# Optimization experiments

Measured on AMD Instinct MI355X. Metric: run time of the kernel, lower is better.

The kernel has to match this reference:

```python
import jax, jax.numpy as jnp
import numpy as np

N, D, IN_DIM, H, L = 20000, 32, 3, 64, 3


def _lstm_agg(h_nodes, nbr_sorted, W_ih, W_hh, b_ih, b_hh):
    """Batched LSTM over each node's (sorted) neighbor sequence; returns final hidden state h_T."""
    n = h_nodes.shape[0]
    hidden = W_hh.shape[1]

    def step(carry, idx):
        h, c = carry
        x = h_nodes[idx]                                     # [N, in_d] irregular gather
        gates = x @ W_ih.T + h @ W_hh.T + b_ih + b_hh        # [N, 4H], torch gate order i,f,g,o
        i_g, f_g, g_g, o_g = jnp.split(gates, 4, axis=-1)
        c = jax.nn.sigmoid(f_g) * c + jax.nn.sigmoid(i_g) * jnp.tanh(g_g)
        h = jax.nn.sigmoid(o_g) * jnp.tanh(c)
        return (h, c), None

    init = (jnp.zeros((n, hidden), h_nodes.dtype), jnp.zeros((n, hidden), h_nodes.dtype))
    (h_T, _), _ = jax.lax.scan(step, init, nbr_sorted.T)      # scan over D neighbor slots
    return h_T


def _layer(h, nbr_sorted, W_ih, W_hh, b_ih, b_hh, Wl, bl):
    agg = _lstm_agg(h, nbr_sorted, W_ih, W_hh, b_ih, b_hh)    # [N, H]
    comb = jnp.concatenate([h, agg], axis=-1)                 # [N, in_d + H]
    return jax.nn.relu(comb @ Wl.T + bl)


def _forward(node_features, nbr, params, W_out, b_out):
    nbr_sorted = jnp.sort(nbr, axis=1)   # permutation-invariant ordering (Eq. 9)
    h = node_features
    for p in params:
        h = _layer(h, nbr_sorted, *p)
    return (h @ W_out.T + b_out).squeeze(-1)   # [N] per-node log-likelihood scores


def setup_inputs():
    key = jax.random.key(0)
    ks = jax.random.split(key, 40)
    inp = {}
    inp["node_features"] = jax.random.normal(ks[0], (N, IN_DIM), jnp.float32)
    inp["nbr"] = jax.random.randint(ks[1], (N, D), 0, N, jnp.int32)
    k = 2
    s = 1.0 / np.sqrt(H)
    for l in range(L):
        in_d = IN_DIM if l == 0 else H
        inp[f"W_ih{l}"] = (jax.random.normal(ks[k], (4 * H, in_d)) * (1.0 / np.sqrt(in_d))).astype(jnp.float32); k += 1
        inp[f"W_hh{l}"] = (jax.random.normal(ks[k], (4 * H, H)) * s).astype(jnp.float32); k += 1
        inp[f"b_ih{l}"] = (jax.random.normal(ks[k], (4 * H,)) * s).astype(jnp.float32); k += 1
        inp[f"b_hh{l}"] = (jax.random.normal(ks[k], (4 * H,)) * s).astype(jnp.float32); k += 1
        inp[f"Wl{l}"] = (jax.random.normal(ks[k], (H, in_d + H)) * (1.0 / np.sqrt(in_d + H))).astype(jnp.float32); k += 1
        inp[f"bl{l}"] = (jax.random.normal(ks[k], (H,)) * s).astype(jnp.float32); k += 1
    inp["W_out"] = (jax.random.normal(ks[k], (1, H)) * s).astype(jnp.float32); k += 1
    inp["b_out"] = jnp.zeros((1,), jnp.float32)
    return inp


def reference(node_features, nbr, W_ih0, W_hh0, b_ih0, b_hh0, Wl0, bl0, W_ih1, W_hh1, b_ih1, b_hh1, Wl1, bl1, W_ih2, W_hh2, b_ih2, b_hh2, Wl2, bl2, W_out, b_out):
    params = [
        (W_ih0, W_hh0, b_ih0, b_hh0, Wl0, bl0),
        (W_ih1, W_hh1, b_ih1, b_hh1, Wl1, bl1),
        (W_ih2, W_hh2, b_ih2, b_hh2, Wl2, bl2),
    ]
    return _forward(node_features, nbr, params, W_out, b_out)
```

## Files before the change

kernel.cpp:

```cpp
#include <hip/hip_runtime.h>
#include <hip/hip_bf16.h>

#define NN 20000
#define NG 1250
#define LOG2E 1.44269504088896f
#define TWOLOG2E 2.88539008177793f

typedef __attribute__((ext_vector_type(8))) short short8;
typedef __attribute__((ext_vector_type(4))) float floatx4;

__device__ __forceinline__ floatx4 MF(short8 a, short8 b, floatx4 c) {
    return __builtin_amdgcn_mfma_f32_16x16x32_bf16(a, b, c, 0, 0, 0);
}
__device__ __forceinline__ float ex2(float x) { return __builtin_amdgcn_exp2f(x); }
__device__ __forceinline__ float rcp(float x) { return __builtin_amdgcn_rcpf(x); }
__device__ __forceinline__ unsigned short bf16r(float x) {
    return __builtin_bit_cast(unsigned short, __float2bfloat16(x));
}
__device__ __forceinline__ void lds_barrier() {
    asm volatile("s_waitcnt lgkmcnt(0)\n\ts_barrier" ::: "memory");
}
__device__ __forceinline__ int rowswz(int L) {
    return L ^ (((L >> 4) & 1) << 1) ^ ((L >> 3) & 1);
}

__global__ void sort_nbrs_kernel(const int* __restrict__ nbr, int* __restrict__ nbrT) {
    int n = blockIdx.x * blockDim.x + threadIdx.x;
    if (n >= NN) return;
    int v[32];
    const int4* src = (const int4*)(nbr + n * 32);
    #pragma unroll
    for (int i = 0; i < 8; i++) {
        int4 t = src[i];
        v[4*i] = t.x; v[4*i+1] = t.y; v[4*i+2] = t.z; v[4*i+3] = t.w;
    }
    #pragma unroll
    for (int k = 2; k <= 32; k <<= 1)
        #pragma unroll
        for (int j = k >> 1; j > 0; j >>= 1)
            #pragma unroll
            for (int i = 0; i < 32; i++) {
                int ixj = i ^ j;
                if (ixj > i) {
                    bool up = (i & k) == 0;
                    int a = v[i], b = v[ixj];
                    bool sw = up ? (a > b) : (a < b);
                    if (sw) { v[i] = b; v[ixj] = a; }
                }
            }
    int g = n >> 4, m = n & 15;
    int base = g * 512 + m;
    #pragma unroll
    for (int t = 0; t < 32; t++) nbrT[base + t * 16] = v[t];
}

#define PREP_TOT (49152 + 49152 + 12288 + 12288 + 768 + 640000)
__global__ void prep_kernel(const float* __restrict__ x,
    const float* __restrict__ Wih0, const float* __restrict__ Whh0,
    const float* __restrict__ bih0, const float* __restrict__ bhh0, const float* __restrict__ Wl0,
    const float* __restrict__ Wih1, const float* __restrict__ Whh1,
    const float* __restrict__ bih1, const float* __restrict__ bhh1, const float* __restrict__ Wl1,
    const float* __restrict__ Wih2, const float* __restrict__ Whh2,
    const float* __restrict__ bih2, const float* __restrict__ bhh2, const float* __restrict__ Wl2,
    unsigned short* __restrict__ Wih_p, unsigned short* __restrict__ Whh_p,
    unsigned short* __restrict__ Wlx_p, unsigned short* __restrict__ Wlh_p,
    float* __restrict__ bsum, unsigned short* __restrict__ x32)
{
    for (int i = blockIdx.x * 256 + threadIdx.x; i < PREP_TOT; i += gridDim.x * 256) {
        int j = i;
        if (j < 49152) {
            int l = j >> 14, e = j & 16383;
            if (l == 0) {
                if (e < 8192) {
                    int col = e >> 5, k = e & 31;
                    float sc = (col >= 128 && col < 192) ? TWOLOG2E : LOG2E;
                    float v = (k < 3) ? Wih0[col*3 + k] * sc : 0.f;
                    Wih_p[e] = bf16r(v);
                }
            } else {
                int col = e >> 6, k = e & 63;
                const float* W = (l == 1) ? Wih1 : Wih2;
                float sc = (col >= 128 && col < 192) ? TWOLOG2E : LOG2E;
                Wih_p[l*16384 + e] = bf16r(W[col*64 + k] * sc);
            }
            continue;
        }
        j -= 49152;
        if (j < 49152) {
            int l = j >> 14, e = j & 16383;
            int col = e >> 6, k = e & 63;
            const float* W = (l == 0) ? Whh0 : ((l == 1) ? Whh1 : Whh2);
            float sc = (col >= 128 && col < 192) ? TWOLOG2E : LOG2E;
            Whh_p[l*16384 + e] = bf16r(W[col*64 + k] * sc);
            continue;
        }
        j -= 49152;
        if (j < 12288) {
            int l = j >> 12, e = j & 4095;
            if (l == 0) {
                if (e < 2048) {
                    int col = e >> 5, k = e & 31;
                    float v = (k < 3) ? Wl0[col*67 + k] : 0.f;
                    Wlx_p[e] = bf16r(v);
                }
            } else {
                int col = e >> 6, k = e & 63;
                const float* W = (l == 1) ? Wl1 : Wl2;
                Wlx_p[l*4096 + e] = bf16r(W[col*128 + k]);
            }
            continue;
        }
        j -= 12288;
        if (j < 12288) {
            int l = j >> 12, e = j & 4095;
            int col = e >> 6, k = e & 63;
            float v = (l == 0) ? Wl0[col*67 + 3 + k]
                               : ((l == 1) ? Wl1 : Wl2)[col*128 + 64 + k];
            Wlh_p[l*4096 + e] = bf16r(v);
            continue;
        }
        j -= 12288;
        if (j < 768) {
            int l = j >> 8, col = j & 255;
            const float* bi = (l == 0) ? bih0 : ((l == 1) ? bih1 : bih2);
            const float* bh = (l == 0) ? bhh0 : ((l == 1) ? bhh1 : bhh2);
            float sc = (col >= 128 && col < 192) ? TWOLOG2E : LOG2E;
            bsum[l*256 + col] = (bi[col] + bh[col]) * sc;
            continue;
        }
        j -= 768;
        {
            int n = j >> 5, k = j & 31;
            x32[j] = bf16r((k < 3) ? x[n*3 + k] : 0.f);
        }
    }
}

template<int XKC, int LASTL>
__global__ __launch_bounds__(256, 3)
void lstm_mfma_kernel(const unsigned short* __restrict__ xsrc,
                      const int* __restrict__ nbrT,
                      const unsigned short* __restrict__ Wih,
                      const unsigned short* __restrict__ Whh,
                      const float* __restrict__ bsum,
                      const unsigned short* __restrict__ Wlx,
                      const unsigned short* __restrict__ Wlh,
                      const float* __restrict__ bl,
                      const float* __restrict__ W_out,
                      const float* __restrict__ b_out,
                      void* __restrict__ hout)
{
    __shared__ unsigned short sA[2][1024];
    __shared__ float sRed[64];

    const int w    = threadIdx.x >> 6;
    const int lane = threadIdx.x & 63;
    const int q    = lane >> 4;
    const int c    = lane & 15;
    const int XS   = XKC * 32;

    const int g = blockIdx.x;
    const int node0 = g * 16;
    const int* nbg = nbrT + g * 512;

    short8 fWih[4][XKC];
    short8 fWhh[4][2];
    float  biasv[4];
    #pragma unroll
    for (int t4 = 0; t4 < 4; t4++) {
        int col = 64*t4 + 16*w + c;
        biasv[t4] = bsum[col];
        #pragma unroll
        for (int kc = 0; kc < XKC; kc++)
            fWih[t4][kc] = *(const short8*)(Wih + col*XS + kc*32 + q*8);
        #pragma unroll
        for (int kc = 0; kc < 2; kc++)
            fWhh[t4][kc] = *(const short8*)(Whh + col*64 + kc*32 + q*8);
    }

    float cst[4] = {0.f, 0.f, 0.f, 0.f};
    short8 hA[2] = {};

    int idx_cur = nbg[c];
    int idx_nxt = nbg[16 + c];
    short8 xg[XKC];
    #pragma unroll
    for (int kc = 0; kc < XKC; kc++)
        xg[kc] = *(const short8*)(xsrc + (long)idx_cur * XS + kc*32 + q*8);

    #pragma unroll 1
    for (int t = 0; t < 32; t++) {
        floatx4 acc[4];
        #pragma unroll
        for (int t4 = 0; t4 < 4; t4++) {
            floatx4 a; a[0] = biasv[t4]; a[1] = biasv[t4]; a[2] = biasv[t4]; a[3] = biasv[t4];
            acc[t4] = a;
        }
        if (t > 0) {
            #pragma unroll
            for (int t4 = 0; t4 < 4; t4++) {
                acc[t4] = MF(hA[0], fWhh[t4][0], acc[t4]);
                acc[t4] = MF(hA[1], fWhh[t4][1], acc[t4]);
            }
        }
        #pragma unroll
        for (int t4 = 0; t4 < 4; t4++)
            #pragma unroll
            for (int kc = 0; kc < XKC; kc++)
                acc[t4] = MF(xg[kc], fWih[t4][kc], acc[t4]);

        if (t < 31) {
            #pragma unroll
            for (int kc = 0; kc < XKC; kc++)
                xg[kc] = *(const short8*)(xsrc + (long)idx_nxt * XS + kc*32 + q*8);
            int tn = (t + 2 < 32) ? t + 2 : 31;
            idx_nxt = nbg[tn*16 + c];
        }

        unsigned short* sAb = sA[t & 1];
        const int u = 16*w + c;
        #pragma unroll
        for (int r = 0; r < 4; r++) {
            float gi = acc[0][r], gf = acc[1][r], gg = acc[2][r], go = acc[3][r];
            float ei = ex2(-gi);
            float ef = ex2(-gf);
            float eo = ex2(-go);
            float eg = ex2(-__builtin_fabsf(gg));
            float iG = __builtin_copysignf(1.f - eg, gg) * rcp((1.f + ei) * (1.f + eg));
            float cm = fmaf(cst[r], rcp(1.f + ef), iG);
            cst[r] = cm;
            float ec = ex2(-TWOLOG2E * __builtin_fabsf(cm));
            float h  = __builtin_copysignf(1.f - ec, cm) * rcp((1.f + eo) * (1.f + ec));
            int row = (4*q + r) + 16*(u >> 3);
            sAb[rowswz(row)*8 + (u & 7)] = bf16r(h);
        }
        lds_barrier();
        hA[0] = *(const short8*)(sA[t & 1] + rowswz(lane)*8);
        hA[1] = *(const short8*)(sA[t & 1] + 512 + rowswz(lane)*8);
    }

    const int col = 16*w + c;
    short8 fx[XKC], fh[2];
    float blv = bl[col];
    #pragma unroll
    for (int kc = 0; kc < XKC; kc++)
        fx[kc] = *(const short8*)(Wlx + col*XS + kc*32 + q*8);
    fh[0] = *(const short8*)(Wlh + col*64 + q*8);
    fh[1] = *(const short8*)(Wlh + col*64 + 32 + q*8);
    short8 hin[XKC];
    #pragma unroll
    for (int kc = 0; kc < XKC; kc++)
        hin[kc] = *(const short8*)(xsrc + (long)(node0 + c) * XS + kc*32 + q*8);

    floatx4 a; a[0] = blv; a[1] = blv; a[2] = blv; a[3] = blv;
    #pragma unroll
    for (int kc = 0; kc < XKC; kc++) a = MF(hin[kc], fx[kc], a);
    a = MF(hA[0], fh[0], a);
    a = MF(hA[1], fh[1], a);

    if (!LASTL) {
        #pragma unroll
        for (int r = 0; r < 4; r++)
            ((unsigned short*)hout)[(node0 + 4*q + r) * 64 + col] = bf16r(fmaxf(a[r], 0.f));
    } else {
        float wo = W_out[col];
        float p[4];
        #pragma unroll
        for (int r = 0; r < 4; r++) p[r] = fmaxf(a[r], 0.f) * wo;
        #pragma unroll
        for (int d = 1; d < 16; d <<= 1) {
            #pragma unroll
            for (int r = 0; r < 4; r++) p[r] += __shfl_xor(p[r], d);
        }
        if (c == 0) {
            #pragma unroll
            for (int r = 0; r < 4; r++) sRed[w*16 + 4*q + r] = p[r];
        }
        lds_barrier();
        if (w == 0 && lane < 16)
            ((float*)hout)[node0 + lane] =
                sRed[lane] + sRed[16 + lane] + sRed[32 + lane] + sRed[48 + lane] + b_out[0];
    }
}

extern "C" void kernel_launch(void* const* d_in, const int* in_sizes, int n_in,
                              void* d_out, int out_size, void* d_ws, size_t ws_size,
                              hipStream_t stream) {
    (void)in_sizes; (void)n_in; (void)out_size; (void)ws_size;
    const float* node_features = (const float*)d_in[0];
    const int*   nbr           = (const int*)d_in[1];
    const float* Wih[3] = {(const float*)d_in[2],  (const float*)d_in[8],  (const float*)d_in[14]};
    const float* Whh[3] = {(const float*)d_in[3],  (const float*)d_in[9],  (const float*)d_in[15]};
    const float* bih[3] = {(const float*)d_in[4],  (const float*)d_in[10], (const float*)d_in[16]};
    const float* bhh[3] = {(const float*)d_in[5],  (const float*)d_in[11], (const float*)d_in[17]};
    const float* Wl[3]  = {(const float*)d_in[6],  (const float*)d_in[12], (const float*)d_in[18]};
    const float* bl[3]  = {(const float*)d_in[7],  (const float*)d_in[13], (const float*)d_in[19]};
    const float* W_out  = (const float*)d_in[20];
    const float* b_out  = (const float*)d_in[21];

    char* ws = (char*)d_ws;
    int*            nbrT  = (int*)ws;
    unsigned short* x32   = (unsigned short*)(ws + 2560000);
    unsigned short* hb1   = (unsigned short*)(ws + 3840000);
    unsigned short* hb2   = (unsigned short*)(ws + 6400000);
    unsigned short* Wih_p = (unsigned short*)(ws + 8960000);
    unsigned short* Whh_p = (unsigned short*)(ws + 9058304);
    unsigned short* Wlx_p = (unsigned short*)(ws + 9156608);
    unsigned short* Wlh_p = (unsigned short*)(ws + 9181184);
    float*          bsum  = (float*)(ws + 9205760);

    prep_kernel<<<1024, 256, 0, stream>>>(node_features,
        Wih[0], Whh[0], bih[0], bhh[0], Wl[0],
        Wih[1], Whh[1], bih[1], bhh[1], Wl[1],
        Wih[2], Whh[2], bih[2], bhh[2], Wl[2],
        Wih_p, Whh_p, Wlx_p, Wlh_p, bsum, x32);
    sort_nbrs_kernel<<<(NN + 255) / 256, 256, 0, stream>>>(nbr, nbrT);

    lstm_mfma_kernel<1, 0><<<NG, 256, 0, stream>>>(x32, nbrT,
        Wih_p,         Whh_p,         bsum,       Wlx_p,        Wlh_p,        bl[0],
        nullptr, nullptr, hb1);
    lstm_mfma_kernel<2, 0><<<NG, 256, 0, stream>>>(hb1, nbrT,
        Wih_p + 16384, Whh_p + 16384, bsum + 256, Wlx_p + 4096, Wlh_p + 4096, bl[1],
        nullptr, nullptr, hb2);
    lstm_mfma_kernel<2, 1><<<NG, 256, 0, stream>>>(hb2, nbrT,
        Wih_p + 32768, Whh_p + 32768, bsum + 512, Wlx_p + 8192, Wlh_p + 8192, bl[2],
        W_out, b_out, (float*)d_out);
}
```

Before: 293.4 us.

## Process two node groups per LSTM block and merge sort into prep kernel

Each LSTM block now handles two independent 16-node groups and interleaves their MFMA chains, gathers and gate math. This gives more instruction-level parallelism to hide the serial recurrence latency and halves the grid. The neighbor sort is folded into the prep kernel as extra blocks, which removes one launch. The cost is higher register pressure under launch_bounds(256,3), and with 625 blocks some CUs may be left idle.

```diff
diff --git a/kernel.cpp b/kernel.cpp
--- a/kernel.cpp
+++ b/kernel.cpp
@@ -3,8 +3,11 @@
 
 #define NN 20000
 #define NG 1250
+#define NB 625
 #define LOG2E 1.44269504088896f
 #define TWOLOG2E 2.88539008177793f
+#define SORT_BLOCKS 79
+#define PREP_BLOCKS 1024
 
 typedef __attribute__((ext_vector_type(8))) short short8;
 typedef __attribute__((ext_vector_type(4))) float floatx4;
@@ -24,38 +27,9 @@
     return L ^ (((L >> 4) & 1) << 1) ^ ((L >> 3) & 1);
 }
 
-__global__ void sort_nbrs_kernel(const int* __restrict__ nbr, int* __restrict__ nbrT) {
-    int n = blockIdx.x * blockDim.x + threadIdx.x;
-    if (n >= NN) return;
-    int v[32];
-    const int4* src = (const int4*)(nbr + n * 32);
-    #pragma unroll
-    for (int i = 0; i < 8; i++) {
-        int4 t = src[i];
-        v[4*i] = t.x; v[4*i+1] = t.y; v[4*i+2] = t.z; v[4*i+3] = t.w;
-    }
-    #pragma unroll
-    for (int k = 2; k <= 32; k <<= 1)
-        #pragma unroll
-        for (int j = k >> 1; j > 0; j >>= 1)
-            #pragma unroll
-            for (int i = 0; i < 32; i++) {
-                int ixj = i ^ j;
-                if (ixj > i) {
-                    bool up = (i & k) == 0;
-                    int a = v[i], b = v[ixj];
-                    bool sw = up ? (a > b) : (a < b);
-                    if (sw) { v[i] = b; v[ixj] = a; }
-                }
-            }
-    int g = n >> 4, m = n & 15;
-    int base = g * 512 + m;
-    #pragma unroll
-    for (int t = 0; t < 32; t++) nbrT[base + t * 16] = v[t];
-}
-
 #define PREP_TOT (49152 + 49152 + 12288 + 12288 + 768 + 640000)
-__global__ void prep_kernel(const float* __restrict__ x,
+__global__ void prep_sort_kernel(const float* __restrict__ x,
+    const int* __restrict__ nbr, int* __restrict__ nbrT,
     const float* __restrict__ Wih0, const float* __restrict__ Whh0,
     const float* __restrict__ bih0, const float* __restrict__ bhh0, const float* __restrict__ Wl0,
     const float* __restrict__ Wih1, const float* __restrict__ Whh1,
@@ -66,7 +40,39 @@
     unsigned short* __restrict__ Wlx_p, unsigned short* __restrict__ Wlh_p,
     float* __restrict__ bsum, unsigned short* __restrict__ x32)
 {
-    for (int i = blockIdx.x * 256 + threadIdx.x; i < PREP_TOT; i += gridDim.x * 256) {
+    if (blockIdx.x < SORT_BLOCKS) {
+        int n = blockIdx.x * 256 + threadIdx.x;
+        if (n >= NN) return;
+        int v[32];
+        const int4* src = (const int4*)(nbr + n * 32);
+        #pragma unroll
+        for (int i = 0; i < 8; i++) {
+            int4 t = src[i];
+            v[4*i] = t.x; v[4*i+1] = t.y; v[4*i+2] = t.z; v[4*i+3] = t.w;
+        }
+        #pragma unroll
+        for (int k = 2; k <= 32; k <<= 1)
+            #pragma unroll
+            for (int j = k >> 1; j > 0; j >>= 1)
+                #pragma unroll
+                for (int i = 0; i < 32; i++) {
+                    int ixj = i ^ j;
+                    if (ixj > i) {
+                        bool up = (i & k) == 0;
+                        int a = v[i], b = v[ixj];
+                        bool sw = up ? (a > b) : (a < b);
+                        if (sw) { v[i] = b; v[ixj] = a; }
+                    }
+                }
+        int g = n >> 4, m = n & 15;
+        int base = g * 512 + m;
+        #pragma unroll
+        for (int t = 0; t < 32; t++) nbrT[base + t * 16] = v[t];
+        return;
+    }
+
+    for (int i = (blockIdx.x - SORT_BLOCKS) * 256 + threadIdx.x; i < PREP_TOT;
+         i += PREP_BLOCKS * 256) {
         int j = i;
         if (j < 49152) {
             int l = j >> 14, e = j & 16383;
@@ -150,8 +156,8 @@
                       const float* __restrict__ b_out,
                       void* __restrict__ hout)
 {
-    __shared__ unsigned short sA[2][1024];
-    __shared__ float sRed[64];
+    __shared__ unsigned short sA[2][2][1024];
+    __shared__ float sRed[2][64];
 
     const int w    = threadIdx.x >> 6;
     const int lane = threadIdx.x & 63;
@@ -159,9 +165,9 @@
     const int c    = lane & 15;
     const int XS   = XKC * 32;
 
-    const int g = blockIdx.x;
-    const int node0 = g * 16;
-    const int* nbg = nbrT + g * 512;
+    const int g0 = blockIdx.x * 2;
+    const int node0[2] = { g0 * 16, g0 * 16 + 16 };
+    const int* nbg[2]  = { nbrT + g0 * 512, nbrT + g0 * 512 + 512 };
 
     short8 fWih[4][XKC];
     short8 fWhh[4][2];
@@ -178,65 +184,84 @@
             fWhh[t4][kc] = *(const short8*)(Whh + col*64 + kc*32 + q*8);
     }
 
-    float cst[4] = {0.f, 0.f, 0.f, 0.f};
-    short8 hA[2] = {};
-
-    int idx_cur = nbg[c];
-    int idx_nxt = nbg[16 + c];
-    short8 xg[XKC];
+    float cst[2][4] = {};
+    short8 hA[2][2] = {};
+
+    int idx_nxt[2];
+    short8 xg[2][XKC];
     #pragma unroll
-    for (int kc = 0; kc < XKC; kc++)
-        xg[kc] = *(const short8*)(xsrc + (long)idx_cur * XS + kc*32 + q*8);
+    for (int gi = 0; gi < 2; gi++) {
+        int ic = nbg[gi][c];
+        idx_nxt[gi] = nbg[gi][16 + c];
+        #pragma unroll
+        for (int kc = 0; kc < XKC; kc++)
+            xg[gi][kc] = *(const short8*)(xsrc + (long)ic * XS + kc*32 + q*8);
+    }
 
     #pragma unroll 1
     for (int t = 0; t < 32; t++) {
-        floatx4 acc[4];
-        #pragma unroll
-        for (int t4 = 0; t4 < 4; t4++) {
-            floatx4 a; a[0] = biasv[t4]; a[1] = biasv[t4]; a[2] = biasv[t4]; a[3] = biasv[t4];
-            acc[t4] = a;
-        }
+        floatx4 acc[2][4];
+        #pragma unroll
+        for (int gi = 0; gi < 2; gi++)
+            #pragma unroll
+            for (int t4 = 0; t4 < 4; t4++) {
+                floatx4 a; a[0] = biasv[t4]; a[1] = biasv[t4]; a[2] = biasv[t4]; a[3] = biasv[t4];
+                acc[gi][t4] = a;
+            }
         if (t > 0) {
             #pragma unroll
-            for (int t4 = 0; t4 < 4; t4++) {
-                acc[t4] = MF(hA[0], fWhh[t4][0], acc[t4]);
-                acc[t4] = MF(hA[1], fWhh[t4][1], acc[t4]);
-            }
+            for (int t4 = 0; t4 < 4; t4++)
+                #pragma unroll
+                for (int gi = 0; gi < 2; gi++) {
+                    acc[gi][t4] = MF(hA[gi][0], fWhh[t4][0], acc[gi][t4]);
+                    acc[gi][t4] = MF(hA[gi][1], fWhh[t4][1], acc[gi][t4]);
+                }
         }
         #pragma unroll
         for (int t4 = 0; t4 < 4; t4++)
             #pragma unroll
-            for (int kc = 0; kc < XKC; kc++)
-                acc[t4] = MF(xg[kc], fWih[t4][kc], acc[t4]);
+            for (int gi = 0; gi < 2; gi++)
+                #pragma unroll
+                for (int kc = 0; kc < XKC; kc++)
+                    acc[gi][t4] = MF(xg[gi][kc], fWih[t4][kc], acc[gi][t4]);
 
         if (t < 31) {
-            #pragma unroll
-            for (int kc = 0; kc < XKC; kc++)
-                xg[kc] = *(const short8*)(xsrc + (long)idx_nxt * XS + kc*32 + q*8);
             int tn = (t + 2 < 32) ? t + 2 : 31;
-            idx_nxt = nbg[tn*16 + c];
-        }
-
-        unsigned short* sAb = sA[t & 1];
+            #pragma unroll
+            for (int gi = 0; gi < 2; gi++) {
+                #pragma unroll
+                for (int kc = 0; kc < XKC; kc++)
+                    xg[gi][kc] = *(const short8*)(xsrc + (long)idx_nxt[gi] * XS + kc*32 + q*8);
+                idx_nxt[gi] = nbg[gi][tn*16 + c];
+            }
+        }
+
         const int u = 16*w + c;
         #pragma unroll
-        for (int r = 0; r < 4; r++) {
-            float gi = acc[0][r], gf = acc[1][r], gg = acc[2][r], go = acc[3][r];
-            float ei = ex2(-gi);
-            float ef = ex2(-gf);
-            float eo = ex2(-go);
-            float eg = ex2(-__builtin_fabsf(gg));
-            float iG = __builtin_copysignf(1.f - eg, gg) * rcp((1.f + ei) * (1.f + eg));
-            float cm = fmaf(cst[r], rcp(1.f + ef), iG);
-            cst[r] = cm;
-            float ec = ex2(-TWOLOG2E * __builtin_fabsf(cm));
-            float h  = __builtin_copysignf(1.f - ec, cm) * rcp((1.f + eo) * (1.f + ec));
-            int row = (4*q + r) + 16*(u >> 3);
-            sAb[rowswz(row)*8 + (u & 7)] = bf16r(h);
+        for (int gi = 0; gi < 2; gi++) {
+            unsigned short* sAb = &sA[gi][t & 1][0];
+            #pragma unroll
+            for (int r = 0; r < 4; r++) {
+                float gv = acc[gi][0][r], gf = acc[gi][1][r], gg = acc[gi][2][r], go = acc[gi][3][r];
+                float ei = ex2(-gv);
+                float ef = ex2(-gf);
+                float eo = ex2(-go);
+                float eg = ex2(-__builtin_fabsf(gg));
+                float iG = __builtin_copysignf(1.f - eg, gg) * rcp((1.f + ei) * (1.f + eg));
+                float cm = fmaf(cst[gi][r], rcp(1.f + ef), iG);
+                cst[gi][r] = cm;
+                float ec = ex2(-TWOLOG2E * __builtin_fabsf(cm));
+                float h  = __builtin_copysignf(1.f - ec, cm) * rcp((1.f + eo) * (1.f + ec));
+                int row = (4*q + r) + 16*(u >> 3);
+                sAb[rowswz(row)*8 + (u & 7)] = bf16r(h);
+            }
         }
         lds_barrier();
-        hA[0] = *(const short8*)(sA[t & 1] + rowswz(lane)*8);
-        hA[1] = *(const short8*)(sA[t & 1] + 512 + rowswz(lane)*8);
+        #pragma unroll
+        for (int gi = 0; gi < 2; gi++) {
+            hA[gi][0] = *(const short8*)(&sA[gi][t & 1][0] + rowswz(lane)*8);
+            hA[gi][1] = *(const short8*)(&sA[gi][t & 1][0] + 512 + rowswz(lane)*8);
+        }
     }
 
     const int col = 16*w + c;
@@ -247,39 +272,46 @@
         fx[kc] = *(const short8*)(Wlx + col*XS + kc*32 + q*8);
     fh[0] = *(const short8*)(Wlh + col*64 + q*8);
     fh[1] = *(const short8*)(Wlh + col*64 + 32 + q*8);
-    short8 hin[XKC];
+
     #pragma unroll
-    for (int kc = 0; kc < XKC; kc++)
-        hin[kc] = *(const short8*)(xsrc + (long)(node0 + c) * XS + kc*32 + q*8);
-
-    floatx4 a; a[0] = blv; a[1] = blv; a[2] = blv; a[3] = blv;
-    #pragma unroll
-    for (int kc = 0; kc < XKC; kc++) a = MF(hin[kc], fx[kc], a);
-    a = MF(hA[0], fh[0], a);
-    a = MF(hA[1], fh[1], a);
-
-    if (!LASTL) {
-        #pragma unroll
-        for (int r = 0; r < 4; r++)
-            ((unsigned short*)hout)[(node0 + 4*q + r) * 64 + col] = bf16r(fmaxf(a[r], 0.f));
-    } else {
-        float wo = W_out[col];
-        float p[4];
-        #pragma unroll
-        for (int r = 0; r < 4; r++) p[r] = fmaxf(a[r], 0.f) * wo;
-        #pragma unroll
-        for (int d = 1; d < 16; d <<= 1) {
-            #pragma unroll
-            for (int r = 0; r < 4; r++) p[r] += __shfl_xor(p[r], d);
-        }
-        if (c == 0) {
-            #pragma unroll
-            for (int r = 0; r < 4; r++) sRed[w*16 + 4*q + r] = p[r];
-        }
+    for (int gi = 0; gi < 2; gi++) {
+        short8 hin[XKC];
+        #pragma unroll
+        for (int kc = 0; kc < XKC; kc++)
+            hin[kc] = *(const short8*)(xsrc + (long)(node0[gi] + c) * XS + kc*32 + q*8);
+
+        floatx4 a; a[0] = blv; a[1] = blv; a[2] = blv; a[3] = blv;
+        #pragma unroll
+        for (int kc = 0; kc < XKC; kc++) a = MF(hin[kc], fx[kc], a);
+        a = MF(hA[gi][0], fh[0], a);
+        a = MF(hA[gi][1], fh[1], a);
+
+        if (!LASTL) {
+            #pragma unroll
+            for (int r = 0; r < 4; r++)
+                ((unsigned short*)hout)[(node0[gi] + 4*q + r) * 64 + col] = bf16r(fmaxf(a[r], 0.f));
+        } else {
+            float wo = W_out[col];
+            float p[4];
+            #pragma unroll
+            for (int r = 0; r < 4; r++) p[r] = fmaxf(a[r], 0.f) * wo;
+            #pragma unroll
+            for (int d = 1; d < 16; d <<= 1) {
+                #pragma unroll
+                for (int r = 0; r < 4; r++) p[r] += __shfl_xor(p[r], d);
+            }
+            if (c == 0) {
+                #pragma unroll
+                for (int r = 0; r < 4; r++) sRed[gi][w*16 + 4*q + r] = p[r];
+            }
+        }
+    }
+    if (LASTL) {
         lds_barrier();
-        if (w == 0 && lane < 16)
-            ((float*)hout)[node0 + lane] =
-                sRed[lane] + sRed[16 + lane] + sRed[32 + lane] + sRed[48 + lane] + b_out[0];
+        if (w < 2 && lane < 16)
+            ((float*)hout)[node0[w] + lane] =
+                sRed[w][lane] + sRed[w][16 + lane] + sRed[w][32 + lane] + sRed[w][48 + lane]
+                + b_out[0];
     }
 }
 
@@ -309,20 +341,20 @@
     unsigned short* Wlh_p = (unsigned short*)(ws + 9181184);
     float*          bsum  = (float*)(ws + 9205760);
 
-    prep_kernel<<<1024, 256, 0, stream>>>(node_features,
+    prep_sort_kernel<<<SORT_BLOCKS + PREP_BLOCKS, 256, 0, stream>>>(node_features,
+        nbr, nbrT,
         Wih[0], Whh[0], bih[0], bhh[0], Wl[0],
         Wih[1], Whh[1], bih[1], bhh[1], Wl[1],
         Wih[2], Whh[2], bih[2], bhh[2], Wl[2],
         Wih_p, Whh_p, Wlx_p, Wlh_p, bsum, x32);
-    sort_nbrs_kernel<<<(NN + 255) / 256, 256, 0, stream>>>(nbr, nbrT);
-
-    lstm_mfma_kernel<1, 0><<<NG, 256, 0, stream>>>(x32, nbrT,
+
+    lstm_mfma_kernel<1, 0><<<NB, 256, 0, stream>>>(x32, nbrT,
         Wih_p,         Whh_p,         bsum,       Wlx_p,        Wlh_p,        bl[0],
         nullptr, nullptr, hb1);
-    lstm_mfma_kernel<2, 0><<<NG, 256, 0, stream>>>(hb1, nbrT,
+    lstm_mfma_kernel<2, 0><<<NB, 256, 0, stream>>>(hb1, nbrT,
         Wih_p + 16384, Whh_p + 16384, bsum + 256, Wlx_p + 4096, Wlh_p + 4096, bl[1],
         nullptr, nullptr, hb2);
-    lstm_mfma_kernel<2, 1><<<NG, 256, 0, stream>>>(hb2, nbrT,
+    lstm_mfma_kernel<2, 1><<<NB, 256, 0, stream>>>(hb2, nbrT,
         Wih_p + 32768, Whh_p + 32768, bsum + 512, Wlx_p + 8192, Wlh_p + 8192, bl[2],
         W_out, b_out, (float*)d_out);
 }
```

Measured after the change: 332.8 us. 13.4% more time.

## Software-pipeline input projection across LSTM steps and merge sort into prep kernel

Applied to the files above, without the earlier changes.

Moves the input-to-hidden MFMA products for step t+1 into step t, after the gate math and before the barrier, using double-buffered accumulators, with the loop unrolled by two. The recurrent critical path then only holds the hidden-state MFMAs, and gather prefetch runs one step further ahead. It also folds the neighbor sort kernel into the prep kernel via block partitioning to drop one launch, and merges two reciprocals in the gate math into one. The cost is more registers for the extra accumulators, which may reduce occupancy.

```diff
diff --git a/kernel.cpp b/kernel.cpp
--- a/kernel.cpp
+++ b/kernel.cpp
@@ -5,6 +5,8 @@
 #define NG 1250
 #define LOG2E 1.44269504088896f
 #define TWOLOG2E 2.88539008177793f
+#define SORT_BLOCKS 79
+#define PREP_BLOCKS 1024
 
 typedef __attribute__((ext_vector_type(8))) short short8;
 typedef __attribute__((ext_vector_type(4))) float floatx4;
@@ -24,38 +26,9 @@
     return L ^ (((L >> 4) & 1) << 1) ^ ((L >> 3) & 1);
 }
 
-__global__ void sort_nbrs_kernel(const int* __restrict__ nbr, int* __restrict__ nbrT) {
-    int n = blockIdx.x * blockDim.x + threadIdx.x;
-    if (n >= NN) return;
-    int v[32];
-    const int4* src = (const int4*)(nbr + n * 32);
-    #pragma unroll
-    for (int i = 0; i < 8; i++) {
-        int4 t = src[i];
-        v[4*i] = t.x; v[4*i+1] = t.y; v[4*i+2] = t.z; v[4*i+3] = t.w;
-    }
-    #pragma unroll
-    for (int k = 2; k <= 32; k <<= 1)
-        #pragma unroll
-        for (int j = k >> 1; j > 0; j >>= 1)
-            #pragma unroll
-            for (int i = 0; i < 32; i++) {
-                int ixj = i ^ j;
-                if (ixj > i) {
-                    bool up = (i & k) == 0;
-                    int a = v[i], b = v[ixj];
-                    bool sw = up ? (a > b) : (a < b);
-                    if (sw) { v[i] = b; v[ixj] = a; }
-                }
-            }
-    int g = n >> 4, m = n & 15;
-    int base = g * 512 + m;
-    #pragma unroll
-    for (int t = 0; t < 32; t++) nbrT[base + t * 16] = v[t];
-}
-
 #define PREP_TOT (49152 + 49152 + 12288 + 12288 + 768 + 640000)
-__global__ void prep_kernel(const float* __restrict__ x,
+__global__ void prep_sort_kernel(const float* __restrict__ x,
+    const int* __restrict__ nbr, int* __restrict__ nbrT,
     const float* __restrict__ Wih0, const float* __restrict__ Whh0,
     const float* __restrict__ bih0, const float* __restrict__ bhh0, const float* __restrict__ Wl0,
     const float* __restrict__ Wih1, const float* __restrict__ Whh1,
@@ -66,7 +39,39 @@
     unsigned short* __restrict__ Wlx_p, unsigned short* __restrict__ Wlh_p,
     float* __restrict__ bsum, unsigned short* __restrict__ x32)
 {
-    for (int i = blockIdx.x * 256 + threadIdx.x; i < PREP_TOT; i += gridDim.x * 256) {
+    if (blockIdx.x < SORT_BLOCKS) {
+        int n = blockIdx.x * 256 + threadIdx.x;
+        if (n >= NN) return;
+        int v[32];
+        const int4* src = (const int4*)(nbr + n * 32);
+        #pragma unroll
+        for (int i = 0; i < 8; i++) {
+            int4 t = src[i];
+            v[4*i] = t.x; v[4*i+1] = t.y; v[4*i+2] = t.z; v[4*i+3] = t.w;
+        }
+        #pragma unroll
+        for (int k = 2; k <= 32; k <<= 1)
+            #pragma unroll
+            for (int j = k >> 1; j > 0; j >>= 1)
+                #pragma unroll
+                for (int i = 0; i < 32; i++) {
+                    int ixj = i ^ j;
+                    if (ixj > i) {
+                        bool up = (i & k) == 0;
+                        int a = v[i], b = v[ixj];
+                        bool sw = up ? (a > b) : (a < b);
+                        if (sw) { v[i] = b; v[ixj] = a; }
+                    }
+                }
+        int g = n >> 4, m = n & 15;
+        int base = g * 512 + m;
+        #pragma unroll
+        for (int t = 0; t < 32; t++) nbrT[base + t * 16] = v[t];
+        return;
+    }
+
+    for (int i = (blockIdx.x - SORT_BLOCKS) * 256 + threadIdx.x; i < PREP_TOT;
+         i += PREP_BLOCKS * 256) {
         int j = i;
         if (j < 49152) {
             int l = j >> 14, e = j & 16383;
@@ -178,68 +183,91 @@
             fWhh[t4][kc] = *(const short8*)(Whh + col*64 + kc*32 + q*8);
     }
 
-    float cst[4] = {0.f, 0.f, 0.f, 0.f};
+    float  cst[4] = {0.f, 0.f, 0.f, 0.f};
     short8 hA[2] = {};
-
-    int idx_cur = nbg[c];
-    int idx_nxt = nbg[16 + c];
+    const int u = 16*w + c;
+
     short8 xg[XKC];
-    #pragma unroll
-    for (int kc = 0; kc < XKC; kc++)
-        xg[kc] = *(const short8*)(xsrc + (long)idx_cur * XS + kc*32 + q*8);
-
-    #pragma unroll 1
-    for (int t = 0; t < 32; t++) {
-        floatx4 acc[4];
-        #pragma unroll
-        for (int t4 = 0; t4 < 4; t4++) {
-            floatx4 a; a[0] = biasv[t4]; a[1] = biasv[t4]; a[2] = biasv[t4]; a[3] = biasv[t4];
-            acc[t4] = a;
-        }
+    {
+        int idx0 = nbg[c];
+        #pragma unroll
+        for (int kc = 0; kc < XKC; kc++)
+            xg[kc] = *(const short8*)(xsrc + (long)idx0 * XS + kc*32 + q*8);
+    }
+    floatx4 accA[4], accB[4];
+    #pragma unroll
+    for (int t4 = 0; t4 < 4; t4++) {
+        floatx4 a; a[0] = biasv[t4]; a[1] = biasv[t4]; a[2] = biasv[t4]; a[3] = biasv[t4];
+        accA[t4] = a;
+    }
+    #pragma unroll
+    for (int t4 = 0; t4 < 4; t4++)
+        #pragma unroll
+        for (int kc = 0; kc < XKC; kc++)
+            accA[t4] = MF(xg[kc], fWih[t4][kc], accA[t4]);
+    {
+        int idx1 = nbg[16 + c];
+        #pragma unroll
+        for (int kc = 0; kc < XKC; kc++)
+            xg[kc] = *(const short8*)(xsrc + (long)idx1 * XS + kc*32 + q*8);
+    }
+    int idx_nxt = nbg[32 + c];
+
+    auto STEP = [&](int t, floatx4 (&cur)[4], floatx4 (&nxt)[4]) {
         if (t > 0) {
             #pragma unroll
             for (int t4 = 0; t4 < 4; t4++) {
-                acc[t4] = MF(hA[0], fWhh[t4][0], acc[t4]);
-                acc[t4] = MF(hA[1], fWhh[t4][1], acc[t4]);
+                cur[t4] = MF(hA[0], fWhh[t4][0], cur[t4]);
+                cur[t4] = MF(hA[1], fWhh[t4][1], cur[t4]);
             }
         }
-        #pragma unroll
-        for (int t4 = 0; t4 < 4; t4++)
-            #pragma unroll
-            for (int kc = 0; kc < XKC; kc++)
-                acc[t4] = MF(xg[kc], fWih[t4][kc], acc[t4]);
-
-        if (t < 31) {
-            #pragma unroll
-            for (int kc = 0; kc < XKC; kc++)
-                xg[kc] = *(const short8*)(xsrc + (long)idx_nxt * XS + kc*32 + q*8);
-            int tn = (t + 2 < 32) ? t + 2 : 31;
-            idx_nxt = nbg[tn*16 + c];
-        }
-
         unsigned short* sAb = sA[t & 1];
-        const int u = 16*w + c;
         #pragma unroll
         for (int r = 0; r < 4; r++) {
-            float gi = acc[0][r], gf = acc[1][r], gg = acc[2][r], go = acc[3][r];
+            float gi = cur[0][r], gf = cur[1][r], gg = cur[2][r], go = cur[3][r];
             float ei = ex2(-gi);
             float ef = ex2(-gf);
             float eo = ex2(-go);
             float eg = ex2(-__builtin_fabsf(gg));
-            float iG = __builtin_copysignf(1.f - eg, gg) * rcp((1.f + ei) * (1.f + eg));
-            float cm = fmaf(cst[r], rcp(1.f + ef), iG);
+            float P  = (1.f + ei) * (1.f + eg);
+            float R  = rcp(P * (1.f + ef));
+            float iG = __builtin_copysignf(1.f - eg, gg) * ((1.f + ef) * R);
+            float cm = fmaf(cst[r], P * R, iG);
             cst[r] = cm;
             float ec = ex2(-TWOLOG2E * __builtin_fabsf(cm));
             float h  = __builtin_copysignf(1.f - ec, cm) * rcp((1.f + eo) * (1.f + ec));
             int row = (4*q + r) + 16*(u >> 3);
             sAb[rowswz(row)*8 + (u & 7)] = bf16r(h);
         }
+        if (t < 31) {
+            #pragma unroll
+            for (int t4 = 0; t4 < 4; t4++) {
+                floatx4 a; a[0] = biasv[t4]; a[1] = biasv[t4]; a[2] = biasv[t4]; a[3] = biasv[t4];
+                nxt[t4] = a;
+            }
+            #pragma unroll
+            for (int t4 = 0; t4 < 4; t4++)
+                #pragma unroll
+                for (int kc = 0; kc < XKC; kc++)
+                    nxt[t4] = MF(xg[kc], fWih[t4][kc], nxt[t4]);
+            #pragma unroll
+            for (int kc = 0; kc < XKC; kc++)
+                xg[kc] = *(const short8*)(xsrc + (long)idx_nxt * XS + kc*32 + q*8);
+            int tn = (t + 3 < 32) ? t + 3 : 31;
+            idx_nxt = nbg[tn*16 + c];
+        }
         lds_barrier();
         hA[0] = *(const short8*)(sA[t & 1] + rowswz(lane)*8);
         hA[1] = *(const short8*)(sA[t & 1] + 512 + rowswz(lane)*8);
-    }
-
-    const int col = 16*w + c;
+    };
+
+    #pragma unroll 1
+    for (int tt = 0; tt < 16; ++tt) {
+        STEP(2*tt,     accA, accB);
+        STEP(2*tt + 1, accB, accA);
+    }
+
+    const int col = u;
     short8 fx[XKC], fh[2];
     float blv = bl[col];
     #pragma unroll
@@ -309,12 +337,12 @@
     unsigned short* Wlh_p = (unsigned short*)(ws + 9181184);
     float*          bsum  = (float*)(ws + 9205760);
 
-    prep_kernel<<<1024, 256, 0, stream>>>(node_features,
+    prep_sort_kernel<<<SORT_BLOCKS + PREP_BLOCKS, 256, 0, stream>>>(node_features,
+        nbr, nbrT,
         Wih[0], Whh[0], bih[0], bhh[0], Wl[0],
         Wih[1], Whh[1], bih[1], bhh[1], Wl[1],
         Wih[2], Whh[2], bih[2], bhh[2], Wl[2],
         Wih_p, Whh_p, Wlx_p, Wlh_p, bsum, x32);
-    sort_nbrs_kernel<<<(NN + 255) / 256, 256, 0, stream>>>(nbr, nbrT);
 
     lstm_mfma_kernel<1, 0><<<NG, 256, 0, stream>>>(x32, nbrT,
         Wih_p,         Whh_p,         bsum,       Wlx_p,        Wlh_p,        bl[0],
```

New measurement: 294.1 us. About the same (+0.3%).
